# Kernel tuning notes

Measured on AMD Instinct MI355X. Metric: run time of the kernel, lower is better.

The kernel has to match this reference:

```python
import jax, jax.numpy as jnp
import numpy as np
import math

NEG_INF = -1e9
B, Q, M, P, HID, H, S = 4, 512, 512, 128, 1024, 16, 64
R = M + Q            # 1024, key length
POSLEN = M + 2 * Q   # 1536


def rel_shift(x):
    # x: [N, H, Q, Rp] -> relative-shifted, same shape
    n, h, q, rp = x.shape
    padded = jnp.pad(x, ((0, 0), (0, 0), (0, 0), (1, 0)))
    return padded.reshape(n, h, rp + 1, q)[:, :, 1:].reshape(n, h, q, rp)


def _attention(query, token_mask, key_content, value, key_position,
               segment_encoding, segment_matrix,
               content_bias, position_bias, segment_bias):
    # query: [N,Q,H,S]; key_content/value: [N,R,H,S]; key_position: [N,Rp,H,S]
    r = key_content.shape[1]
    content_att = jnp.einsum('nqhs,nrhs->nhqr', query + content_bias, key_content)
    position_att = jnp.einsum('nqhs,nrhs->nhqr', query + position_bias, key_position)
    position_att = rel_shift(position_att)[..., 1:1 + r]
    segment_att = jnp.einsum('nqhs,ghs->nhqg', query + segment_bias, segment_encoding)
    # select same-segment (g=1) vs diff-segment (g=0) logit per (q, r) pair
    segment_att = jnp.where(segment_matrix[:, None],           # [N,1,Q,R]
                            segment_att[..., 1:],              # [N,H,Q,1]
                            segment_att[..., :1])
    scale = 1.0 / math.sqrt(float(S))
    logits = (content_att + position_att + segment_att) * scale
    logits = logits + token_mask * NEG_INF
    weights = jax.nn.softmax(logits, axis=3)
    return jnp.einsum('nhqr,nrhs->nqhs', weights, value)


def setup_inputs() -> dict:
    key = jax.random.key(0)
    ks = jax.random.split(key, 16)
    sc = 0.05
    content_inputs = jax.random.normal(ks[0], (B, Q, HID), jnp.float32)
    query_inputs = jax.random.normal(ks[1], (B, P, HID), jnp.float32)
    position_encoding = jax.random.normal(ks[2], (B, POSLEN, HID), jnp.float32)
    segment_encoding = jax.random.normal(ks[3], (2, H, S), jnp.float32) * sc
    segment_matrix = jax.random.randint(ks[4], (B, Q, R), 0, 2) > 0
    # one-hot target mapping: P distinct target positions per batch row
    tpos = jax.vmap(lambda k: jax.random.permutation(k, Q)[:P])(jax.random.split(ks[5], B))
    target_mapping = jax.nn.one_hot(tpos, Q, dtype=jnp.float32)  # [B,P,Q]
    # causal-style permutation masks (1 = masked)
    causal = (jnp.arange(R)[None, :] > (jnp.arange(Q)[:, None] + M)).astype(jnp.float32)
    content_mask = jnp.broadcast_to(causal[None, None], (B, 1, Q, R))
    diag = jnp.pad(jnp.eye(Q, dtype=jnp.float32), ((0, 0), (M, 0)))
    query_mask = jnp.broadcast_to(jnp.minimum(causal + diag, 1.0)[None, None], (B, 1, Q, R))
    content_bias = jax.random.normal(ks[6], (H, S), jnp.float32) * sc
    position_bias = jax.random.normal(ks[7], (H, S), jnp.float32) * sc
    segment_bias = jax.random.normal(ks[8], (H, S), jnp.float32) * sc
    mems = jax.random.normal(ks[9], (B, M, HID), jnp.float32)
    wsc = 1.0 / math.sqrt(HID)
    Wq = jax.random.normal(ks[10], (HID, H, S), jnp.float32) * wsc
    Wkc = jax.random.normal(ks[11], (HID, H, S), jnp.float32) * wsc
    Wv = jax.random.normal(ks[12], (HID, H, S), jnp.float32) * wsc
    Wkp = jax.random.normal(ks[13], (HID, H, S), jnp.float32) * wsc
    Wo = jax.random.normal(ks[14], (H, S, HID), jnp.float32) * wsc
    return dict(content_inputs=content_inputs, query_inputs=query_inputs,
                position_encoding=position_encoding, segment_encoding=segment_encoding,
                segment_matrix=segment_matrix, target_mapping=target_mapping,
                content_mask=content_mask, query_mask=query_mask,
                content_bias=content_bias, position_bias=position_bias,
                segment_bias=segment_bias, mems=mems,
                Wq=Wq, Wkc=Wkc, Wv=Wv, Wkp=Wkp, Wo=Wo)


def reference(content_inputs, query_inputs, position_encoding, segment_encoding,
              segment_matrix, target_mapping, content_mask, query_mask,
              content_bias, position_bias, segment_bias, mems,
              Wq, Wkc, Wv, Wkp, Wo):
    split = lambda x, w: jnp.einsum('nld,dhs->nlhs', x, w)
    merge = lambda x, w: jnp.einsum('nlhs,hsd->nld', x, w)
    contexts = jnp.concatenate([mems, content_inputs], axis=1)  # [B,R,HID]
    key_content = split(contexts, Wkc)
    value = split(contexts, Wv)
    key_position = split(position_encoding, Wkp)
    attn = lambda q, m: _attention(q, m, key_content, value, key_position,
                                   segment_encoding, segment_matrix,
                                   content_bias, position_bias, segment_bias)
    # content stream
    q_c = split(content_inputs, Wq)
    content_outputs = merge(attn(q_c, content_mask), Wo)
    # query stream, scattered to target positions via one-hot target_mapping
    q_q = split(query_inputs, Wq)                               # [B,P,H,S]
    q_q = jnp.einsum('nphs,npq->nqhs', q_q, target_mapping)     # [B,Q,H,S]
    query_outputs = attn(q_q, query_mask)
    query_outputs = jnp.einsum('nqhs,npq->nphs', query_outputs, target_mapping)
    query_outputs = merge(query_outputs, Wo)
    return content_outputs, query_outputs
```

## Files before the change

kernel.cpp:

```cpp
#include <hip/hip_runtime.h>
#include <hip/hip_bf16.h>
#include <math.h>

#define B_ 4
#define Q_ 512
#define M_ 512
#define P_ 128
#define HID_ 1024
#define H_ 16
#define S_ 64
#define R_ 1024
#define POSLEN_ 1536

typedef short bf16x8 __attribute__((ext_vector_type(8)));
typedef float f32x4 __attribute__((ext_vector_type(4)));
typedef unsigned int u32;
typedef unsigned long long u64;

__device__ __forceinline__ ushort f2bf(float f) {
    u32 u = __float_as_uint(f);
    u32 r = (u + 0x7fffu + ((u >> 16) & 1u)) >> 16;
    return (ushort)r;
}
__device__ __forceinline__ float bf2f(ushort s) {
    return __uint_as_float(((u32)s) << 16);
}
__device__ __forceinline__ void gload16(void* l, const void* g) {
    __builtin_amdgcn_global_load_lds(
        (const __attribute__((address_space(1))) u32*)g,
        (__attribute__((address_space(3))) u32*)l, 16, 0, 0);
}

__global__ void find_tpos_k(const float* __restrict__ tm, int* __restrict__ tpos) {
    int i = blockIdx.x * blockDim.x + threadIdx.x;
    if (i >= B_ * P_) return;
    const float* row = tm + (size_t)i * Q_;
    int q = 0;
    for (int j = 0; j < Q_; ++j) q = (row[j] > 0.5f) ? j : q;
    tpos[i] = q;
}

__global__ __launch_bounds__(256) void cvt_all(
    const float* __restrict__ content, const float* __restrict__ mems,
    const float* __restrict__ posenc,  const float* __restrict__ query,
    ushort* __restrict__ ctx, ushort* __restrict__ pos,
    ushort* __restrict__ cont, ushort* __restrict__ qry)
{
    int v = blockIdx.x * 256 + threadIdx.x;
    const float* src;
    ushort* dst;
    if (v < 524288) {
        int row = v >> 7, c8 = v & 127;
        int n = row >> 10, l = row & 1023;
        src = (l < M_) ? mems + ((size_t)(n * M_ + l)) * 1024 + c8 * 8
                       : content + ((size_t)(n * Q_ + (l - M_))) * 1024 + c8 * 8;
        dst = ctx + (size_t)v * 8;
    } else if (v < 1310720) {
        int u = v - 524288;
        src = posenc + (size_t)u * 8; dst = pos + (size_t)u * 8;
    } else if (v < 1572864) {
        int u = v - 1310720;
        src = content + (size_t)u * 8; dst = cont + (size_t)u * 8;
    } else {
        int u = v - 1572864;
        src = query + (size_t)u * 8; dst = qry + (size_t)u * 8;
    }
    float4 a = *(const float4*)src;
    float4 b = *(const float4*)(src + 4);
    ushort4 o0 = {f2bf(a.x), f2bf(a.y), f2bf(a.z), f2bf(a.w)};
    ushort4 o1 = {f2bf(b.x), f2bf(b.y), f2bf(b.z), f2bf(b.w)};
    *(ushort4*)dst = o0;
    *(ushort4*)(dst + 4) = o1;
}

__global__ __launch_bounds__(256) void transpose5(
    const float* W0, const float* W1, const float* W2, const float* W3, const float* W4,
    ushort* T0, ushort* T1, ushort* T2, ushort* T3, ushort* T4)
{
    __shared__ float t[32][33];
    const float* W; ushort* T;
    switch (blockIdx.z) {
        case 0: W = W0; T = T0; break;
        case 1: W = W1; T = T1; break;
        case 2: W = W2; T = T2; break;
        case 3: W = W3; T = T3; break;
        default: W = W4; T = T4; break;
    }
    int bx = blockIdx.x * 32, by = blockIdx.y * 32;
    int tx = threadIdx.x & 31, ty = threadIdx.x >> 5;
    #pragma unroll
    for (int i = 0; i < 32; i += 8)
        t[ty + i][tx] = W[(size_t)(by + ty + i) * 1024 + bx + tx];
    __syncthreads();
    #pragma unroll
    for (int i = 0; i < 32; i += 8)
        T[(size_t)(bx + ty + i) * 1024 + by + tx] = f2bf(t[tx][ty + i]);
}

__global__ __launch_bounds__(256) void seg_prep(const float* __restrict__ segenc,
                                                const float* __restrict__ cb,
                                                const float* __restrict__ sb,
                                                ushort* __restrict__ seg_bf,
                                                float* __restrict__ segc) {
    for (int t = threadIdx.x; t < 16 * 16 * 64; t += 256) {
        int h = t >> 10, g = (t >> 6) & 15, s = t & 63;
        float v = (g < 2) ? segenc[(size_t)(g * 16 + h) * 64 + s] : 0.f;
        seg_bf[t] = f2bf(v);
    }
    if (threadIdx.x < 32) {
        int h = threadIdx.x >> 1, g = threadIdx.x & 1;
        float acc = 0.f;
        for (int s = 0; s < 64; ++s)
            acc += (sb[h * 64 + s] - cb[h * 64 + s]) * segenc[(size_t)(g * 16 + h) * 64 + s];
        segc[h * 2 + g] = acc;
    }
}

__global__ __launch_bounds__(256) void pack_seg(const int* __restrict__ seg, u64* __restrict__ out) {
    int idx = blockIdx.x * 256 + threadIdx.x;
    u64 m = __ballot(seg[idx] > 0);
    if ((threadIdx.x & 63) == 0) out[idx >> 6] = m;
}

__global__ __launch_bounds__(256) void proj_all(
    const ushort* __restrict__ ctx, const ushort* __restrict__ pos,
    const ushort* __restrict__ cont, const ushort* __restrict__ qry,
    const ushort* __restrict__ Wkc_t, const ushort* __restrict__ Wv_t,
    const ushort* __restrict__ Wkp_t, const ushort* __restrict__ Wq_t,
    ushort* __restrict__ KC, ushort* __restrict__ Vt, ushort* __restrict__ KP,
    ushort* __restrict__ Qccb, ushort* __restrict__ Qcpb,
    ushort* __restrict__ Qqcb, ushort* __restrict__ Qqpb,
    const float* __restrict__ cbias, const float* __restrict__ pbias)
{
    __shared__ ushort As[128 * 64];
    __shared__ ushort Bs[64 * 64];
    const int y = blockIdx.y;
    const ushort *A, *Bt;
    ushort *O1, *O2 = nullptr;
    const float *b1 = nullptr, *b2 = nullptr;
    int LROWS, MODE, m0;
    if (y < 32)       { A = ctx;  Bt = Wkc_t; O1 = KC;   LROWS = 1024; MODE = 1; m0 = y * 128; }
    else if (y < 64)  { A = ctx;  Bt = Wv_t;  O1 = Vt;   LROWS = 1024; MODE = 2; m0 = (y - 32) * 128; }
    else if (y < 112) { A = pos;  Bt = Wkp_t; O1 = KP;   LROWS = 1536; MODE = 1; m0 = (y - 64) * 128; }
    else if (y < 128) { A = cont; Bt = Wq_t;  O1 = Qccb; O2 = Qcpb; b1 = cbias; b2 = pbias; LROWS = 512; MODE = 1; m0 = (y - 112) * 128; }
    else              { A = qry;  Bt = Wq_t;  O1 = Qqcb; O2 = Qqpb; b1 = cbias; b2 = pbias; LROWS = 128; MODE = 1; m0 = (y - 128) * 128; }
    const int nn_blk = m0 / LROWS;
    const int lrbase = m0 - nn_blk * LROWS;

    const int tid = threadIdx.x;
    const int lane = tid & 63, wave = tid >> 6;
    const int l15 = lane & 15, hi = lane >> 4;
    const int wm = wave >> 1, wn = wave & 1;
    const int n0 = blockIdx.x * 64;

    f32x4 acc[4][2];
    #pragma unroll
    for (int i = 0; i < 4; ++i)
        #pragma unroll
        for (int j = 0; j < 2; ++j) acc[i][j] = f32x4{0.f, 0.f, 0.f, 0.f};

    for (int k0 = 0; k0 < 1024; k0 += 64) {
        __syncthreads();
        #pragma unroll
        for (int it = 0; it < 4; ++it) {
            int idx = it * 256 + tid;
            gload16(&As[idx * 8], A + (size_t)(m0 + (idx >> 3)) * 1024 + k0 + (idx & 7) * 8);
        }
        #pragma unroll
        for (int it = 0; it < 2; ++it) {
            int idx = it * 256 + tid;
            gload16(&Bs[idx * 8], Bt + (size_t)(n0 + (idx >> 3)) * 1024 + k0 + (idx & 7) * 8);
        }
        __syncthreads();
        #pragma unroll
        for (int kk = 0; kk < 2; ++kk) {
            const int krd = kk * 32 + hi * 8;
            bf16x8 af[4], bfr[2];
            #pragma unroll
            for (int i = 0; i < 4; ++i)
                af[i] = *(const bf16x8*)&As[(wm * 64 + i * 16 + l15) * 64 + krd];
            #pragma unroll
            for (int j = 0; j < 2; ++j)
                bfr[j] = *(const bf16x8*)&Bs[(wn * 32 + j * 16 + l15) * 64 + krd];
            #pragma unroll
            for (int i = 0; i < 4; ++i)
                #pragma unroll
                for (int j = 0; j < 2; ++j)
                    acc[i][j] = __builtin_amdgcn_mfma_f32_16x16x32_bf16(af[i], bfr[j], acc[i][j], 0, 0, 0);
        }
    }

    #pragma unroll
    for (int i = 0; i < 4; ++i)
        #pragma unroll
        for (int j = 0; j < 2; ++j) {
            int col = n0 + wn * 32 + j * 16 + l15;
            float bb1 = b1 ? b1[col] : 0.f;
            float bb2 = b2 ? b2[col] : 0.f;
            #pragma unroll
            for (int r = 0; r < 4; ++r) {
                int lrow = wm * 64 + i * 16 + hi * 4 + r;
                float v = acc[i][j][r];
                if (MODE == 1) {
                    size_t o = ((size_t)(nn_blk * 16 + (col >> 6)) * LROWS + lrbase + lrow) * 64 + (col & 63);
                    O1[o] = f2bf(v + bb1);
                    if (O2) O2[o] = f2bf(v + bb2);
                } else {
                    int row = m0 + lrow;
                    int nn = row >> 10, rr = row & 1023;
                    O1[((size_t)(nn * 16 + (col >> 6)) * 64 + (col & 63)) * 1024 + rr] = f2bf(v);
                }
            }
        }
}

__global__ __launch_bounds__(256) void oproj(
    const ushort* __restrict__ AOc, const ushort* __restrict__ AOq,
    const ushort* __restrict__ Wo_t, float* __restrict__ out)
{
    __shared__ ushort As[128 * 64];
    __shared__ ushort Bs[64 * 64];
    const int y = blockIdx.y;
    const ushort* A;
    float* C;
    int m0;
    if (y < 16) { A = AOc; C = out; m0 = y * 128; }
    else        { A = AOq; C = out + (size_t)B_ * Q_ * 1024; m0 = (y - 16) * 128; }

    const int tid = threadIdx.x;
    const int lane = tid & 63, wave = tid >> 6;
    const int l15 = lane & 15, hi = lane >> 4;
    const int wm = wave >> 1, wn = wave & 1;
    const int n0 = blockIdx.x * 64;

    f32x4 acc[4][2];
    #pragma unroll
    for (int i = 0; i < 4; ++i)
        #pragma unroll
        for (int j = 0; j < 2; ++j) acc[i][j] = f32x4{0.f, 0.f, 0.f, 0.f};

    for (int k0 = 0; k0 < 1024; k0 += 64) {
        __syncthreads();
        #pragma unroll
        for (int it = 0; it < 4; ++it) {
            int idx = it * 256 + tid;
            gload16(&As[idx * 8], A + (size_t)(m0 + (idx >> 3)) * 1024 + k0 + (idx & 7) * 8);
        }
        #pragma unroll
        for (int it = 0; it < 2; ++it) {
            int idx = it * 256 + tid;
            gload16(&Bs[idx * 8], Wo_t + (size_t)(n0 + (idx >> 3)) * 1024 + k0 + (idx & 7) * 8);
        }
        __syncthreads();
        #pragma unroll
        for (int kk = 0; kk < 2; ++kk) {
            const int krd = kk * 32 + hi * 8;
            bf16x8 af[4], bfr[2];
            #pragma unroll
            for (int i = 0; i < 4; ++i)
                af[i] = *(const bf16x8*)&As[(wm * 64 + i * 16 + l15) * 64 + krd];
            #pragma unroll
            for (int j = 0; j < 2; ++j)
                bfr[j] = *(const bf16x8*)&Bs[(wn * 32 + j * 16 + l15) * 64 + krd];
            #pragma unroll
            for (int i = 0; i < 4; ++i)
                #pragma unroll
                for (int j = 0; j < 2; ++j)
                    acc[i][j] = __builtin_amdgcn_mfma_f32_16x16x32_bf16(af[i], bfr[j], acc[i][j], 0, 0, 0);
        }
    }
    #pragma unroll
    for (int i = 0; i < 4; ++i)
        #pragma unroll
        for (int j = 0; j < 2; ++j) {
            int col = n0 + wn * 32 + j * 16 + l15;
            #pragma unroll
            for (int r = 0; r < 4; ++r) {
                int row = m0 + wm * 64 + i * 16 + hi * 4 + r;
                C[(size_t)row * 1024 + col] = acc[i][j][r];
            }
        }
}

__global__ __launch_bounds__(256) void pa_gemm(const ushort* __restrict__ Qpb,
                                               const ushort* __restrict__ KPb,
                                               ushort* __restrict__ PA) {
    const int tid = threadIdx.x;
    const int lane = tid & 63, w = tid >> 6;
    const int l15 = lane & 15, hi = lane >> 4;
    const int jt = blockIdx.x * 128, nh = blockIdx.y;
    const int p0 = w * 32;

    bf16x8 a[2][2];
    #pragma unroll
    for (int i = 0; i < 2; ++i)
        #pragma unroll
        for (int kk = 0; kk < 2; ++kk)
            a[i][kk] = *(const bf16x8*)(Qpb + ((size_t)(nh * 128 + p0 + i * 16 + l15)) * 64 + kk * 32 + hi * 8);

    #pragma unroll
    for (int jc = 0; jc < 8; ++jc) {
        f32x4 c0 = {0.f,0.f,0.f,0.f}, c1 = {0.f,0.f,0.f,0.f};
        #pragma unroll
        for (int kk = 0; kk < 2; ++kk) {
            bf16x8 b = *(const bf16x8*)(KPb + ((size_t)nh * 1536 + jt + jc * 16 + l15) * 64 + kk * 32 + hi * 8);
            c0 = __builtin_amdgcn_mfma_f32_16x16x32_bf16(a[0][kk], b, c0, 0, 0, 0);
            c1 = __builtin_amdgcn_mfma_f32_16x16x32_bf16(a[1][kk], b, c1, 0, 0, 0);
        }
        #pragma unroll
        for (int r = 0; r < 4; ++r) {
            PA[((size_t)(nh * 128 + p0 + hi * 4 + r)) * 1536 + jt + jc * 16 + l15] = f2bf(c0[r]);
            PA[((size_t)(nh * 128 + p0 + 16 + hi * 4 + r)) * 1536 + jt + jc * 16 + l15] = f2bf(c1[r]);
        }
    }
}

#define EXSC 0.180336879f
#define EXBI -23.0831204f
__global__ __launch_bounds__(128) void attn_uni(
    const ushort* __restrict__ Qccb, const ushort* __restrict__ Qcpb,
    const ushort* __restrict__ Qqcb,
    const ushort* __restrict__ KCb,  const ushort* __restrict__ KPb,
    const ushort* __restrict__ Vtb,  const ushort* __restrict__ segb,
    const float* __restrict__ segc,  const u64* __restrict__ pseg,
    const int* __restrict__ tpos,    const ushort* __restrict__ PA,
    float* __restrict__ Pp)
{
    __shared__ ushort Kt[2][64 * 64];
    __shared__ ushort DlT[2][96 * 34];
    __shared__ ushort Pl[2][32 * 64];

    const int tid = threadIdx.x;
    const int lane = tid & 63, wv = tid >> 6;
    const int l15 = lane & 15, hi = lane >> 4;

    int wg = blockIdx.x + 10 * (blockIdx.y + 32 * blockIdx.z);
    int swz = (wg & 7) * 160 + (wg >> 3);
    const int bx = swz % 10;
    int rem = swz / 10;
    const int gy = rem & 31;
    const int n = rem >> 5;

    const bool ISQ = bx >= 8;
    const int h = gy & 15, half = gy >> 4;
    const int nh = n * 16 + h;
    const int q0w = (ISQ ? (bx - 8) * 64 : bx * 64) + wv * 32;

    ushort* dlt = DlT[wv];
    ushort* pl  = Pl[wv];

    bf16x8 acb[2][2], apb[2][2];
    {
        const ushort* qc = ISQ ? (Qqcb + ((size_t)nh * P_ + q0w) * 64)
                               : (Qccb + ((size_t)nh * Q_ + q0w) * 64);
        #pragma unroll
        for (int i = 0; i < 2; ++i)
            #pragma unroll
            for (int kk = 0; kk < 2; ++kk)
                acb[i][kk] = *(const bf16x8*)(qc + (size_t)(i * 16 + l15) * 64 + kk * 32 + hi * 8);
        if (!ISQ) {
            const ushort* qp = Qcpb + ((size_t)nh * Q_ + q0w) * 64;
            #pragma unroll
            for (int i = 0; i < 2; ++i)
                #pragma unroll
                for (int kk = 0; kk < 2; ++kk)
                    apb[i][kk] = *(const bf16x8*)(qp + (size_t)(i * 16 + l15) * 64 + kk * 32 + hi * 8);
        } else {
            apb[0][0] = acb[0][0]; apb[0][1] = acb[0][1];
            apb[1][0] = acb[1][0]; apb[1][1] = acb[1][1];
        }
    }

    float sd[2][2][4];
    {
        f32x4 sg[2] = {{0.f,0.f,0.f,0.f},{0.f,0.f,0.f,0.f}};
        #pragma unroll
        for (int kk = 0; kk < 2; ++kk) {
            bf16x8 b = *(const bf16x8*)(segb + (size_t)(h * 16 + l15) * 64 + kk * 32 + hi * 8);
            sg[0] = __builtin_amdgcn_mfma_f32_16x16x32_bf16(acb[0][kk], b, sg[0], 0, 0, 0);
            sg[1] = __builtin_amdgcn_mfma_f32_16x16x32_bf16(acb[1][kk], b, sg[1], 0, 0, 0);
        }
        float c0 = segc[h * 2 + 0], c1 = segc[h * 2 + 1];
        #pragma unroll
        for (int i = 0; i < 2; ++i)
            #pragma unroll
            for (int r = 0; r < 4; ++r) {
                int base = (lane & 48) << 2;
                sd[0][i][r] = __int_as_float(__builtin_amdgcn_ds_bpermute(base, __float_as_int(sg[i][r]))) + c0;
                sd[1][i][r] = __int_as_float(__builtin_amdgcn_ds_bpermute(base + 4, __float_as_int(sg[i][r]))) + c1;
            }
    }

    int qg[2][4];
    #pragma unroll
    for (int i = 0; i < 2; ++i)
        #pragma unroll
        for (int r = 0; r < 4; ++r) {
            int p = q0w + i * 16 + hi * 4 + r;
            qg[i][r] = ISQ ? tpos[n * P_ + p] : p;
        }

    f32x4 acc[2][4];
    float psum[2][4] = {};
    #pragma unroll
    for (int i = 0; i < 2; ++i)
        #pragma unroll
        for (int j = 0; j < 4; ++j) acc[i][j] = f32x4{0.f,0.f,0.f,0.f};

    auto stage = [&](int b, int rt) {
        const int r0s = rt * 64;
        #pragma unroll
        for (int it = 0; it < 4; ++it) {
            int e = it * 128 + tid;
            int row = e >> 3;
            int sc = ((e & 7) * 8) ^ ((row & 7) << 3);
            gload16(&Kt[b][e * 8], KCb + ((size_t)nh * R_ + r0s + row) * 64 + sc);
        }
    };

    const int q0top = (ISQ ? (bx - 8) * 64 : bx * 64) + 32;
    const int ntb = ISQ ? 16 : min(16, ((q0top + 543) >> 6) + 1);
    const int nt1 = (ntb + 1) >> 1;
    const int t0 = half ? nt1 : 0;
    const int tmax = half ? ntb : nt1;

    stage(0, t0);
    __syncthreads();
    int buf = 0;

    for (int rt = t0; rt < tmax; ++rt) {
        const int r0 = rt * 64;
        if (rt + 1 < tmax) stage(buf ^ 1, rt + 1);

        const bool skip = !ISQ && (r0 > q0w + 543);
        if (!skip) {
            bf16x8 vf[2][4];
            #pragma unroll
            for (int kk = 0; kk < 2; ++kk)
                #pragma unroll
                for (int dj = 0; dj < 4; ++dj)
                    vf[kk][dj] = *(const bf16x8*)(Vtb + ((size_t)nh * 64 + dj * 16 + l15) * 1024 + r0 + kk * 32 + hi * 8);

            f32x4 s[2][4];
            #pragma unroll
            for (int i = 0; i < 2; ++i)
                #pragma unroll
                for (int fc = 0; fc < 4; ++fc) s[i][fc] = f32x4{0.f,0.f,0.f,0.f};
            #pragma unroll
            for (int kk = 0; kk < 2; ++kk) {
                #pragma unroll
                for (int fc = 0; fc < 4; ++fc) {
                    int krow = fc * 16 + l15;
                    bf16x8 kb = *(const bf16x8*)&Kt[buf][krow * 64 + ((kk * 32 + hi * 8) ^ ((krow & 7) << 3))];
                    s[0][fc] = __builtin_amdgcn_mfma_f32_16x16x32_bf16(acb[0][kk], kb, s[0][fc], 0, 0, 0);
                    s[1][fc] = __builtin_amdgcn_mfma_f32_16x16x32_bf16(acb[1][kk], kb, s[1][fc], 0, 0, 0);
                }
            }

            if (!ISQ) {
                const int jb0 = r0 - q0w + 481;
                #pragma unroll
                for (int t = 0; t < 6; ++t) {
                    f32x4 d0 = {0.f,0.f,0.f,0.f}, d1 = {0.f,0.f,0.f,0.f};
                    #pragma unroll
                    for (int kk = 0; kk < 2; ++kk) {
                        bf16x8 pv = *(const bf16x8*)(KPb + ((size_t)nh * POSLEN_ + jb0 + t * 16 + l15) * 64 + kk * 32 + hi * 8);
                        d0 = __builtin_amdgcn_mfma_f32_16x16x32_bf16(apb[0][kk], pv, d0, 0, 0, 0);
                        d1 = __builtin_amdgcn_mfma_f32_16x16x32_bf16(apb[1][kk], pv, d1, 0, 0, 0);
                    }
                    int jj = (t * 16 + l15) * 34;
                    *(u32*)&dlt[jj + hi * 4]          = (u32)f2bf(d0[0]) | ((u32)f2bf(d0[1]) << 16);
                    *(u32*)&dlt[jj + hi * 4 + 2]      = (u32)f2bf(d0[2]) | ((u32)f2bf(d0[3]) << 16);
                    *(u32*)&dlt[jj + 16 + hi * 4]     = (u32)f2bf(d1[0]) | ((u32)f2bf(d1[1]) << 16);
                    *(u32*)&dlt[jj + 16 + hi * 4 + 2] = (u32)f2bf(d1[2]) | ((u32)f2bf(d1[3]) << 16);
                }
            }

            float pav[2][4][4];
            if (ISQ) {
                #pragma unroll
                for (int i = 0; i < 2; ++i)
                    #pragma unroll
                    for (int fc = 0; fc < 4; ++fc)
                        #pragma unroll
                        for (int r = 0; r < 4; ++r) {
                            int qq = i * 16 + hi * 4 + r;
                            int j = (r0 + fc * 16 + l15) - qg[i][r] + 512;
                            pav[i][fc][r] = bf2f(PA[((size_t)nh * P_ + q0w + qq) * 1536 + j]);
                        }
            }

            #pragma unroll
            for (int i = 0; i < 2; ++i) {
                u64 sw[4];
                #pragma unroll
                for (int r = 0; r < 4; ++r)
                    sw[r] = pseg[((size_t)n * Q_ + qg[i][r]) * 16 + rt];
                #pragma unroll
                for (int fc = 0; fc < 4; ++fc) {
                    #pragma unroll
                    for (int r = 0; r < 4; ++r) {
                        int qq = i * 16 + hi * 4 + r;
                        int rr = fc * 16 + l15;
                        float dval = ISQ ? pav[i][fc][r] : bf2f(dlt[(rr - qq + 31) * 34 + qq]);
                        int sel = (int)((sw[r] >> rr) & 1);
                        float st = s[i][fc][r] + dval + (sel ? sd[1][i][r] : sd[0][i][r]);
                        float v = fmaf(st, EXSC, EXBI);
                        bool masked = ISQ ? ((r0 + rr) >= qg[i][r] + 512)
                                          : ((r0 + rr) > qg[i][r] + 512);
                        v = masked ? -INFINITY : v;
                        float pv = exp2f(v);
                        ushort us = f2bf(pv);
                        psum[i][r] += bf2f(us);
                        int row = i * 16 + hi * 4 + r;
                        int cc = (fc * 16 + l15) ^ ((row & 7) << 3);
                        pl[row * 64 + cc] = us;
                    }
                }
            }

            #pragma unroll
            for (int kk = 0; kk < 2; ++kk) {
                bf16x8 pa[2];
                #pragma unroll
                for (int i = 0; i < 2; ++i) {
                    int row = i * 16 + l15;
                    int cc = (kk * 32 + hi * 8) ^ ((row & 7) << 3);
                    pa[i] = *(const bf16x8*)&pl[row * 64 + cc];
                }
                #pragma unroll
                for (int dj = 0; dj < 4; ++dj) {
                    acc[0][dj] = __builtin_amdgcn_mfma_f32_16x16x32_bf16(pa[0], vf[kk][dj], acc[0][dj], 0, 0, 0);
                    acc[1][dj] = __builtin_amdgcn_mfma_f32_16x16x32_bf16(pa[1], vf[kk][dj], acc[1][dj], 0, 0, 0);
                }
            }
        }
        __syncthreads();
        buf ^= 1;
    }

    #pragma unroll
    for (int i = 0; i < 2; ++i)
        #pragma unroll
        for (int r = 0; r < 4; ++r) {
            #pragma unroll
            for (int d = 1; d < 16; d <<= 1) psum[i][r] += __shfl_xor(psum[i][r], d, 64);
        }

    #pragma unroll
    for (int i = 0; i < 2; ++i)
        #pragma unroll
        for (int r = 0; r < 4; ++r) {
            int qrow = q0w + i * 16 + hi * 4 + r;
            size_t rowg = ISQ ? (32768 + (size_t)nh * P_ + qrow) : ((size_t)nh * Q_ + qrow);
            float* base = Pp + (rowg * 2 + half) * 72;
            #pragma unroll
            for (int dj = 0; dj < 4; ++dj)
                base[dj * 16 + l15] = acc[i][dj][r];
            if (l15 == 0) base[64] = psum[i][r];
        }
}

__global__ __launch_bounds__(256) void combine_k(const float* __restrict__ Pp,
                                                 ushort* __restrict__ AOc,
                                                 ushort* __restrict__ AOq) {
    int idx = blockIdx.x * 256 + threadIdx.x;
    int row = idx >> 6, d = idx & 63;
    const float* b0 = Pp + ((size_t)row * 2 + 0) * 72;
    const float* b1 = b0 + 72;
    float l = b0[64] + b1[64];
    ushort o = f2bf((b0[d] + b1[d]) / l);
    if (row < 32768) {
        int n = row >> 13, h = (row >> 9) & 15, q = row & 511;
        AOc[((size_t)(n * Q_ + q)) * 1024 + h * 64 + d] = o;
    } else {
        int r2 = row - 32768;
        int n = r2 >> 11, h = (r2 >> 7) & 15, p = r2 & 127;
        AOq[((size_t)(n * P_ + p)) * 1024 + h * 64 + d] = o;
    }
}

extern "C" void kernel_launch(void* const* d_in, const int* in_sizes, int n_in,
                              void* d_out, int out_size, void* d_ws, size_t ws_size,
                              hipStream_t stream) {
    const float* content = (const float*)d_in[0];
    const float* query   = (const float*)d_in[1];
    const float* posenc  = (const float*)d_in[2];
    const float* segenc  = (const float*)d_in[3];
    const int*   segmat  = (const int*)d_in[4];
    const float* tmap    = (const float*)d_in[5];
    const float* cbias   = (const float*)d_in[8];
    const float* pbias   = (const float*)d_in[9];
    const float* sbias   = (const float*)d_in[10];
    const float* mems    = (const float*)d_in[11];
    const float* Wq      = (const float*)d_in[12];
    const float* Wkc     = (const float*)d_in[13];
    const float* Wv      = (const float*)d_in[14];
    const float* Wkp     = (const float*)d_in[15];
    const float* Wo      = (const float*)d_in[16];
    float* out = (float*)d_out;

    char* p = (char*)d_ws;
    auto alloc = [&](size_t bytes) { char* r = p; p += (bytes + 255) & ~(size_t)255; return r; };
    ushort* ctx_bf  = (ushort*)alloc((size_t)B_ * R_ * 1024 * 2);
    ushort* pos_bf  = (ushort*)alloc((size_t)B_ * POSLEN_ * 1024 * 2);
    ushort* cont_bf = (ushort*)alloc((size_t)B_ * Q_ * 1024 * 2);
    ushort* qry_bf  = (ushort*)alloc((size_t)B_ * P_ * 1024 * 2);
    ushort* Wq_t    = (ushort*)alloc(1024 * 1024 * 2);
    ushort* Wkc_t   = (ushort*)alloc(1024 * 1024 * 2);
    ushort* Wv_t    = (ushort*)alloc(1024 * 1024 * 2);
    ushort* Wkp_t   = (ushort*)alloc(1024 * 1024 * 2);
    ushort* Wo_t    = (ushort*)alloc(1024 * 1024 * 2);
    ushort* KC_bf   = (ushort*)alloc((size_t)B_ * 16 * R_ * 64 * 2);
    ushort* Vt_bf   = (ushort*)alloc((size_t)B_ * 16 * 64 * R_ * 2);
    ushort* KP_bf   = (ushort*)alloc((size_t)B_ * 16 * POSLEN_ * 64 * 2);
    ushort* Qc_cb   = (ushort*)alloc((size_t)B_ * 16 * Q_ * 64 * 2);
    ushort* Qc_pb   = (ushort*)alloc((size_t)B_ * 16 * Q_ * 64 * 2);
    ushort* Qq_cb   = (ushort*)alloc((size_t)B_ * 16 * P_ * 64 * 2);
    ushort* Qq_pb   = (ushort*)alloc((size_t)B_ * 16 * P_ * 64 * 2);
    ushort* PA_bf   = (ushort*)alloc((size_t)B_ * 16 * P_ * POSLEN_ * 2);
    ushort* AOc_bf  = (ushort*)alloc((size_t)B_ * Q_ * 1024 * 2);
    ushort* AOq_bf  = (ushort*)alloc((size_t)B_ * P_ * 1024 * 2);
    ushort* seg_bf  = (ushort*)alloc(16 * 16 * 64 * 2);
    float*  segc    = (float*)alloc(32 * 4);
    u64*    pseg    = (u64*)alloc((size_t)B_ * Q_ * 16 * 8);
    int*    tpos    = (int*)alloc(B_ * P_ * 4);
    float* Pp = (float*)ctx_bf;

    find_tpos_k<<<2, 256, 0, stream>>>(tmap, tpos);
    cvt_all<<<6400, 256, 0, stream>>>(content, mems, posenc, query,
                                      ctx_bf, pos_bf, cont_bf, qry_bf);
    transpose5<<<dim3(32, 32, 5), 256, 0, stream>>>(Wq, Wkc, Wv, Wkp, Wo,
                                                    Wq_t, Wkc_t, Wv_t, Wkp_t, Wo_t);
    seg_prep<<<1, 256, 0, stream>>>(segenc, cbias, sbias, seg_bf, segc);
    pack_seg<<<8192, 256, 0, stream>>>(segmat, pseg);

    proj_all<<<dim3(16, 132), 256, 0, stream>>>(ctx_bf, pos_bf, cont_bf, qry_bf,
                                                Wkc_t, Wv_t, Wkp_t, Wq_t,
                                                KC_bf, Vt_bf, KP_bf,
                                                Qc_cb, Qc_pb, Qq_cb, Qq_pb,
                                                cbias, pbias);

    pa_gemm<<<dim3(12, 64), 256, 0, stream>>>(Qq_pb, KP_bf, PA_bf);

    attn_uni<<<dim3(10, 32, 4), 128, 0, stream>>>(Qc_cb, Qc_pb, Qq_cb, KC_bf, KP_bf, Vt_bf,
                                                  seg_bf, segc, pseg, tpos, PA_bf, Pp);

    combine_k<<<10240, 256, 0, stream>>>(Pp, AOc_bf, AOq_bf);

    oproj<<<dim3(16, 20), 256, 0, stream>>>(AOc_bf, AOq_bf, Wo_t, out);

    (void)in_sizes; (void)n_in; (void)out_size; (void)ws_size;
}
```

Measured before the change: 317.1 us.

## Widen projection GEMM tiles and split attention into single-wave blocks

The projection and output GEMMs move from 128x64 to 128x128 tiles, giving each wave a 4x4 MFMA block, halving the grid, and reusing each A tile across more output columns. The attention kernel becomes one wave per block with 32 query rows. It drops the LDS-staged, double-buffered K tile and its barriers, loading K fragments straight from global memory. The relative-position band is now kept in fp32 LDS instead of bf16, and per-wave causal tile counts are tighter. The trade-off is more accumulator registers in the GEMMs, fewer GEMM blocks for occupancy, and unstaged global K loads in attention.

```diff
diff --git a/kernel.cpp b/kernel.cpp
--- a/kernel.cpp
+++ b/kernel.cpp
@@ -133,7 +133,7 @@
     const float* __restrict__ cbias, const float* __restrict__ pbias)
 {
     __shared__ ushort As[128 * 64];
-    __shared__ ushort Bs[64 * 64];
+    __shared__ ushort Bs[128 * 64];
     const int y = blockIdx.y;
     const ushort *A, *Bt;
     ushort *O1, *O2 = nullptr;
@@ -151,13 +151,13 @@
     const int lane = tid & 63, wave = tid >> 6;
     const int l15 = lane & 15, hi = lane >> 4;
     const int wm = wave >> 1, wn = wave & 1;
-    const int n0 = blockIdx.x * 64;
-
-    f32x4 acc[4][2];
+    const int n0 = blockIdx.x * 128;
+
+    f32x4 acc[4][4];
     #pragma unroll
     for (int i = 0; i < 4; ++i)
         #pragma unroll
-        for (int j = 0; j < 2; ++j) acc[i][j] = f32x4{0.f, 0.f, 0.f, 0.f};
+        for (int j = 0; j < 4; ++j) acc[i][j] = f32x4{0.f, 0.f, 0.f, 0.f};
 
     for (int k0 = 0; k0 < 1024; k0 += 64) {
         __syncthreads();
@@ -165,27 +165,22 @@
         for (int it = 0; it < 4; ++it) {
             int idx = it * 256 + tid;
             gload16(&As[idx * 8], A + (size_t)(m0 + (idx >> 3)) * 1024 + k0 + (idx & 7) * 8);
-        }
-        #pragma unroll
-        for (int it = 0; it < 2; ++it) {
-            int idx = it * 256 + tid;
             gload16(&Bs[idx * 8], Bt + (size_t)(n0 + (idx >> 3)) * 1024 + k0 + (idx & 7) * 8);
         }
         __syncthreads();
         #pragma unroll
         for (int kk = 0; kk < 2; ++kk) {
             const int krd = kk * 32 + hi * 8;
-            bf16x8 af[4], bfr[2];
-            #pragma unroll
-            for (int i = 0; i < 4; ++i)
-                af[i] = *(const bf16x8*)&As[(wm * 64 + i * 16 + l15) * 64 + krd];
-            #pragma unroll
-            for (int j = 0; j < 2; ++j)
-                bfr[j] = *(const bf16x8*)&Bs[(wn * 32 + j * 16 + l15) * 64 + krd];
+            bf16x8 af[4], bfr[4];
+            #pragma unroll
+            for (int i = 0; i < 4; ++i) {
+                af[i]  = *(const bf16x8*)&As[(wm * 64 + i * 16 + l15) * 64 + krd];
+                bfr[i] = *(const bf16x8*)&Bs[(wn * 64 + i * 16 + l15) * 64 + krd];
+            }
             #pragma unroll
             for (int i = 0; i < 4; ++i)
                 #pragma unroll
-                for (int j = 0; j < 2; ++j)
+                for (int j = 0; j < 4; ++j)
                     acc[i][j] = __builtin_amdgcn_mfma_f32_16x16x32_bf16(af[i], bfr[j], acc[i][j], 0, 0, 0);
         }
     }
@@ -193,8 +188,8 @@
     #pragma unroll
     for (int i = 0; i < 4; ++i)
         #pragma unroll
-        for (int j = 0; j < 2; ++j) {
-            int col = n0 + wn * 32 + j * 16 + l15;
+        for (int j = 0; j < 4; ++j) {
+            int col = n0 + wn * 64 + j * 16 + l15;
             float bb1 = b1 ? b1[col] : 0.f;
             float bb2 = b2 ? b2[col] : 0.f;
             #pragma unroll
@@ -219,7 +214,7 @@
     const ushort* __restrict__ Wo_t, float* __restrict__ out)
 {
     __shared__ ushort As[128 * 64];
-    __shared__ ushort Bs[64 * 64];
+    __shared__ ushort Bs[128 * 64];
     const int y = blockIdx.y;
     const ushort* A;
     float* C;
@@ -231,13 +226,13 @@
     const int lane = tid & 63, wave = tid >> 6;
     const int l15 = lane & 15, hi = lane >> 4;
     const int wm = wave >> 1, wn = wave & 1;
-    const int n0 = blockIdx.x * 64;
-
-    f32x4 acc[4][2];
+    const int n0 = blockIdx.x * 128;
+
+    f32x4 acc[4][4];
     #pragma unroll
     for (int i = 0; i < 4; ++i)
         #pragma unroll
-        for (int j = 0; j < 2; ++j) acc[i][j] = f32x4{0.f, 0.f, 0.f, 0.f};
+        for (int j = 0; j < 4; ++j) acc[i][j] = f32x4{0.f, 0.f, 0.f, 0.f};
 
     for (int k0 = 0; k0 < 1024; k0 += 64) {
         __syncthreads();
@@ -245,35 +240,30 @@
         for (int it = 0; it < 4; ++it) {
             int idx = it * 256 + tid;
             gload16(&As[idx * 8], A + (size_t)(m0 + (idx >> 3)) * 1024 + k0 + (idx & 7) * 8);
-        }
-        #pragma unroll
-        for (int it = 0; it < 2; ++it) {
-            int idx = it * 256 + tid;
             gload16(&Bs[idx * 8], Wo_t + (size_t)(n0 + (idx >> 3)) * 1024 + k0 + (idx & 7) * 8);
         }
         __syncthreads();
         #pragma unroll
         for (int kk = 0; kk < 2; ++kk) {
             const int krd = kk * 32 + hi * 8;
-            bf16x8 af[4], bfr[2];
-            #pragma unroll
-            for (int i = 0; i < 4; ++i)
-                af[i] = *(const bf16x8*)&As[(wm * 64 + i * 16 + l15) * 64 + krd];
-            #pragma unroll
-            for (int j = 0; j < 2; ++j)
-                bfr[j] = *(const bf16x8*)&Bs[(wn * 32 + j * 16 + l15) * 64 + krd];
+            bf16x8 af[4], bfr[4];
+            #pragma unroll
+            for (int i = 0; i < 4; ++i) {
+                af[i]  = *(const bf16x8*)&As[(wm * 64 + i * 16 + l15) * 64 + krd];
+                bfr[i] = *(const bf16x8*)&Bs[(wn * 64 + i * 16 + l15) * 64 + krd];
+            }
             #pragma unroll
             for (int i = 0; i < 4; ++i)
                 #pragma unroll
-                for (int j = 0; j < 2; ++j)
+                for (int j = 0; j < 4; ++j)
                     acc[i][j] = __builtin_amdgcn_mfma_f32_16x16x32_bf16(af[i], bfr[j], acc[i][j], 0, 0, 0);
         }
     }
     #pragma unroll
     for (int i = 0; i < 4; ++i)
         #pragma unroll
-        for (int j = 0; j < 2; ++j) {
-            int col = n0 + wn * 32 + j * 16 + l15;
+        for (int j = 0; j < 4; ++j) {
+            int col = n0 + wn * 64 + j * 16 + l15;
             #pragma unroll
             for (int r = 0; r < 4; ++r) {
                 int row = m0 + wm * 64 + i * 16 + hi * 4 + r;
@@ -317,7 +307,7 @@
 
 #define EXSC 0.180336879f
 #define EXBI -23.0831204f
-__global__ __launch_bounds__(128) void attn_uni(
+__global__ __launch_bounds__(64) void attn_uni(
     const ushort* __restrict__ Qccb, const ushort* __restrict__ Qcpb,
     const ushort* __restrict__ Qqcb,
     const ushort* __restrict__ KCb,  const ushort* __restrict__ KPb,
@@ -326,28 +316,23 @@
     const int* __restrict__ tpos,    const ushort* __restrict__ PA,
     float* __restrict__ Pp)
 {
-    __shared__ ushort Kt[2][64 * 64];
-    __shared__ ushort DlT[2][96 * 34];
-    __shared__ ushort Pl[2][32 * 64];
-
-    const int tid = threadIdx.x;
-    const int lane = tid & 63, wv = tid >> 6;
+    __shared__ float Dlf[96 * 36];
+    __shared__ ushort Pl[32 * 64];
+
+    const int lane = threadIdx.x;
     const int l15 = lane & 15, hi = lane >> 4;
 
-    int wg = blockIdx.x + 10 * (blockIdx.y + 32 * blockIdx.z);
-    int swz = (wg & 7) * 160 + (wg >> 3);
-    const int bx = swz % 10;
-    int rem = swz / 10;
+    int wg = blockIdx.x + 20 * (blockIdx.y + 32 * blockIdx.z);
+    int swz = (wg & 7) * 320 + (wg >> 3);
+    const int bx = swz % 20;
+    int rem = swz / 20;
     const int gy = rem & 31;
     const int n = rem >> 5;
 
-    const bool ISQ = bx >= 8;
+    const bool ISQ = bx >= 16;
     const int h = gy & 15, half = gy >> 4;
     const int nh = n * 16 + h;
-    const int q0w = (ISQ ? (bx - 8) * 64 : bx * 64) + wv * 32;
-
-    ushort* dlt = DlT[wv];
-    ushort* pl  = Pl[wv];
+    const int q0w = (ISQ ? (bx - 16) : bx) * 32;
 
     bf16x8 acb[2][2], apb[2][2];
     {
@@ -407,136 +392,114 @@
         #pragma unroll
         for (int j = 0; j < 4; ++j) acc[i][j] = f32x4{0.f,0.f,0.f,0.f};
 
-    auto stage = [&](int b, int rt) {
-        const int r0s = rt * 64;
-        #pragma unroll
-        for (int it = 0; it < 4; ++it) {
-            int e = it * 128 + tid;
-            int row = e >> 3;
-            int sc = ((e & 7) * 8) ^ ((row & 7) << 3);
-            gload16(&Kt[b][e * 8], KCb + ((size_t)nh * R_ + r0s + row) * 64 + sc);
-        }
-    };
-
-    const int q0top = (ISQ ? (bx - 8) * 64 : bx * 64) + 32;
-    const int ntb = ISQ ? 16 : min(16, ((q0top + 543) >> 6) + 1);
+    const int ntb = ISQ ? 16 : (((q0w + 543) >> 6) + 1);
     const int nt1 = (ntb + 1) >> 1;
     const int t0 = half ? nt1 : 0;
     const int tmax = half ? ntb : nt1;
 
-    stage(0, t0);
-    __syncthreads();
-    int buf = 0;
-
     for (int rt = t0; rt < tmax; ++rt) {
         const int r0 = rt * 64;
-        if (rt + 1 < tmax) stage(buf ^ 1, rt + 1);
-
-        const bool skip = !ISQ && (r0 > q0w + 543);
-        if (!skip) {
-            bf16x8 vf[2][4];
-            #pragma unroll
-            for (int kk = 0; kk < 2; ++kk)
+
+        bf16x8 vf[2][4], kf[2][4];
+        #pragma unroll
+        for (int kk = 0; kk < 2; ++kk)
+            #pragma unroll
+            for (int dj = 0; dj < 4; ++dj)
+                vf[kk][dj] = *(const bf16x8*)(Vtb + ((size_t)nh * 64 + dj * 16 + l15) * 1024 + r0 + kk * 32 + hi * 8);
+        #pragma unroll
+        for (int kk = 0; kk < 2; ++kk)
+            #pragma unroll
+            for (int fc = 0; fc < 4; ++fc)
+                kf[kk][fc] = *(const bf16x8*)(KCb + ((size_t)nh * R_ + r0 + fc * 16 + l15) * 64 + kk * 32 + hi * 8);
+
+        f32x4 s[2][4];
+        #pragma unroll
+        for (int i = 0; i < 2; ++i)
+            #pragma unroll
+            for (int fc = 0; fc < 4; ++fc) s[i][fc] = f32x4{0.f,0.f,0.f,0.f};
+        #pragma unroll
+        for (int kk = 0; kk < 2; ++kk)
+            #pragma unroll
+            for (int fc = 0; fc < 4; ++fc) {
+                s[0][fc] = __builtin_amdgcn_mfma_f32_16x16x32_bf16(acb[0][kk], kf[kk][fc], s[0][fc], 0, 0, 0);
+                s[1][fc] = __builtin_amdgcn_mfma_f32_16x16x32_bf16(acb[1][kk], kf[kk][fc], s[1][fc], 0, 0, 0);
+            }
+
+        if (!ISQ) {
+            const int jb0 = r0 - q0w + 481;
+            #pragma unroll
+            for (int t = 0; t < 6; ++t) {
+                f32x4 d0 = {0.f,0.f,0.f,0.f}, d1 = {0.f,0.f,0.f,0.f};
                 #pragma unroll
-                for (int dj = 0; dj < 4; ++dj)
-                    vf[kk][dj] = *(const bf16x8*)(Vtb + ((size_t)nh * 64 + dj * 16 + l15) * 1024 + r0 + kk * 32 + hi * 8);
-
-            f32x4 s[2][4];
+                for (int kk = 0; kk < 2; ++kk) {
+                    bf16x8 pv = *(const bf16x8*)(KPb + ((size_t)nh * POSLEN_ + jb0 + t * 16 + l15) * 64 + kk * 32 + hi * 8);
+                    d0 = __builtin_amdgcn_mfma_f32_16x16x32_bf16(apb[0][kk], pv, d0, 0, 0, 0);
+                    d1 = __builtin_amdgcn_mfma_f32_16x16x32_bf16(apb[1][kk], pv, d1, 0, 0, 0);
+                }
+                float* wp = &Dlf[(t * 16 + l15) * 36];
+                *(f32x4*)(wp + hi * 4) = d0;
+                *(f32x4*)(wp + 16 + hi * 4) = d1;
+            }
+        }
+
+        float pav[2][4][4];
+        if (ISQ) {
             #pragma unroll
             for (int i = 0; i < 2; ++i)
                 #pragma unroll
-                for (int fc = 0; fc < 4; ++fc) s[i][fc] = f32x4{0.f,0.f,0.f,0.f};
-            #pragma unroll
-            for (int kk = 0; kk < 2; ++kk) {
-                #pragma unroll
-                for (int fc = 0; fc < 4; ++fc) {
-                    int krow = fc * 16 + l15;
-                    bf16x8 kb = *(const bf16x8*)&Kt[buf][krow * 64 + ((kk * 32 + hi * 8) ^ ((krow & 7) << 3))];
-                    s[0][fc] = __builtin_amdgcn_mfma_f32_16x16x32_bf16(acb[0][kk], kb, s[0][fc], 0, 0, 0);
-                    s[1][fc] = __builtin_amdgcn_mfma_f32_16x16x32_bf16(acb[1][kk], kb, s[1][fc], 0, 0, 0);
-                }
-            }
-
-            if (!ISQ) {
-                const int jb0 = r0 - q0w + 481;
-                #pragma unroll
-                for (int t = 0; t < 6; ++t) {
-                    f32x4 d0 = {0.f,0.f,0.f,0.f}, d1 = {0.f,0.f,0.f,0.f};
-                    #pragma unroll
-                    for (int kk = 0; kk < 2; ++kk) {
-                        bf16x8 pv = *(const bf16x8*)(KPb + ((size_t)nh * POSLEN_ + jb0 + t * 16 + l15) * 64 + kk * 32 + hi * 8);
-                        d0 = __builtin_amdgcn_mfma_f32_16x16x32_bf16(apb[0][kk], pv, d0, 0, 0, 0);
-                        d1 = __builtin_amdgcn_mfma_f32_16x16x32_bf16(apb[1][kk], pv, d1, 0, 0, 0);
-                    }
-                    int jj = (t * 16 + l15) * 34;
-                    *(u32*)&dlt[jj + hi * 4]          = (u32)f2bf(d0[0]) | ((u32)f2bf(d0[1]) << 16);
-                    *(u32*)&dlt[jj + hi * 4 + 2]      = (u32)f2bf(d0[2]) | ((u32)f2bf(d0[3]) << 16);
-                    *(u32*)&dlt[jj + 16 + hi * 4]     = (u32)f2bf(d1[0]) | ((u32)f2bf(d1[1]) << 16);
-                    *(u32*)&dlt[jj + 16 + hi * 4 + 2] = (u32)f2bf(d1[2]) | ((u32)f2bf(d1[3]) << 16);
-                }
-            }
-
-            float pav[2][4][4];
-            if (ISQ) {
-                #pragma unroll
-                for (int i = 0; i < 2; ++i)
-                    #pragma unroll
-                    for (int fc = 0; fc < 4; ++fc)
-                        #pragma unroll
-                        for (int r = 0; r < 4; ++r) {
-                            int qq = i * 16 + hi * 4 + r;
-                            int j = (r0 + fc * 16 + l15) - qg[i][r] + 512;
-                            pav[i][fc][r] = bf2f(PA[((size_t)nh * P_ + q0w + qq) * 1536 + j]);
-                        }
-            }
-
-            #pragma unroll
-            for (int i = 0; i < 2; ++i) {
-                u64 sw[4];
-                #pragma unroll
-                for (int r = 0; r < 4; ++r)
-                    sw[r] = pseg[((size_t)n * Q_ + qg[i][r]) * 16 + rt];
-                #pragma unroll
-                for (int fc = 0; fc < 4; ++fc) {
+                for (int fc = 0; fc < 4; ++fc)
                     #pragma unroll
                     for (int r = 0; r < 4; ++r) {
                         int qq = i * 16 + hi * 4 + r;
-                        int rr = fc * 16 + l15;
-                        float dval = ISQ ? pav[i][fc][r] : bf2f(dlt[(rr - qq + 31) * 34 + qq]);
-                        int sel = (int)((sw[r] >> rr) & 1);
-                        float st = s[i][fc][r] + dval + (sel ? sd[1][i][r] : sd[0][i][r]);
-                        float v = fmaf(st, EXSC, EXBI);
-                        bool masked = ISQ ? ((r0 + rr) >= qg[i][r] + 512)
-                                          : ((r0 + rr) > qg[i][r] + 512);
-                        v = masked ? -INFINITY : v;
-                        float pv = exp2f(v);
-                        ushort us = f2bf(pv);
-                        psum[i][r] += bf2f(us);
-                        int row = i * 16 + hi * 4 + r;
-                        int cc = (fc * 16 + l15) ^ ((row & 7) << 3);
-                        pl[row * 64 + cc] = us;
+                        int j = (r0 + fc * 16 + l15) - qg[i][r] + 512;
+                        pav[i][fc][r] = bf2f(PA[((size_t)nh * P_ + q0w + qq) * 1536 + j]);
                     }
+        }
+
+        #pragma unroll
+        for (int i = 0; i < 2; ++i) {
+            u64 sw[4];
+            #pragma unroll
+            for (int r = 0; r < 4; ++r)
+                sw[r] = pseg[((size_t)n * Q_ + qg[i][r]) * 16 + rt];
+            #pragma unroll
+            for (int fc = 0; fc < 4; ++fc) {
+                #pragma unroll
+                for (int r = 0; r < 4; ++r) {
+                    int qq = i * 16 + hi * 4 + r;
+                    int rr = fc * 16 + l15;
+                    float dval = ISQ ? pav[i][fc][r] : Dlf[(rr - qq + 31) * 36 + qq];
+                    int sel = (int)((sw[r] >> rr) & 1);
+                    float st = s[i][fc][r] + dval + (sel ? sd[1][i][r] : sd[0][i][r]);
+                    float v = fmaf(st, EXSC, EXBI);
+                    bool masked = ISQ ? ((r0 + rr) >= qg[i][r] + 512)
+                                      : ((r0 + rr) > qg[i][r] + 512);
+                    v = masked ? -INFINITY : v;
+                    float pv = exp2f(v);
+                    ushort us = f2bf(pv);
+                    psum[i][r] += bf2f(us);
+                    int row = i * 16 + hi * 4 + r;
+                    int cc = (fc * 16 + l15) ^ ((row & 7) << 3);
+                    Pl[row * 64 + cc] = us;
                 }
             }
-
-            #pragma unroll
-            for (int kk = 0; kk < 2; ++kk) {
-                bf16x8 pa[2];
-                #pragma unroll
-                for (int i = 0; i < 2; ++i) {
-                    int row = i * 16 + l15;
-                    int cc = (kk * 32 + hi * 8) ^ ((row & 7) << 3);
-                    pa[i] = *(const bf16x8*)&pl[row * 64 + cc];
-                }
-                #pragma unroll
-                for (int dj = 0; dj < 4; ++dj) {
-                    acc[0][dj] = __builtin_amdgcn_mfma_f32_16x16x32_bf16(pa[0], vf[kk][dj], acc[0][dj], 0, 0, 0);
-                    acc[1][dj] = __builtin_amdgcn_mfma_f32_16x16x32_bf16(pa[1], vf[kk][dj], acc[1][dj], 0, 0, 0);
-                }
-            }
-        }
-        __syncthreads();
-        buf ^= 1;
+        }
+
+        #pragma unroll
+        for (int kk = 0; kk < 2; ++kk) {
+            bf16x8 pa[2];
+            #pragma unroll
+            for (int i = 0; i < 2; ++i) {
+                int row = i * 16 + l15;
+                int cc = (kk * 32 + hi * 8) ^ ((row & 7) << 3);
+                pa[i] = *(const bf16x8*)&Pl[row * 64 + cc];
+            }
+            #pragma unroll
+            for (int dj = 0; dj < 4; ++dj) {
+                acc[0][dj] = __builtin_amdgcn_mfma_f32_16x16x32_bf16(pa[0], vf[kk][dj], acc[0][dj], 0, 0, 0);
+                acc[1][dj] = __builtin_amdgcn_mfma_f32_16x16x32_bf16(pa[1], vf[kk][dj], acc[1][dj], 0, 0, 0);
+            }
+        }
     }
 
     #pragma unroll
@@ -635,20 +598,20 @@
     seg_prep<<<1, 256, 0, stream>>>(segenc, cbias, sbias, seg_bf, segc);
     pack_seg<<<8192, 256, 0, stream>>>(segmat, pseg);
 
-    proj_all<<<dim3(16, 132), 256, 0, stream>>>(ctx_bf, pos_bf, cont_bf, qry_bf,
-                                                Wkc_t, Wv_t, Wkp_t, Wq_t,
-                                                KC_bf, Vt_bf, KP_bf,
-                                                Qc_cb, Qc_pb, Qq_cb, Qq_pb,
-                                                cbias, pbias);
+    proj_all<<<dim3(8, 132), 256, 0, stream>>>(ctx_bf, pos_bf, cont_bf, qry_bf,
+                                               Wkc_t, Wv_t, Wkp_t, Wq_t,
+                                               KC_bf, Vt_bf, KP_bf,
+                                               Qc_cb, Qc_pb, Qq_cb, Qq_pb,
+                                               cbias, pbias);
 
     pa_gemm<<<dim3(12, 64), 256, 0, stream>>>(Qq_pb, KP_bf, PA_bf);
 
-    attn_uni<<<dim3(10, 32, 4), 128, 0, stream>>>(Qc_cb, Qc_pb, Qq_cb, KC_bf, KP_bf, Vt_bf,
-                                                  seg_bf, segc, pseg, tpos, PA_bf, Pp);
+    attn_uni<<<dim3(20, 32, 4), 64, 0, stream>>>(Qc_cb, Qc_pb, Qq_cb, KC_bf, KP_bf, Vt_bf,
+                                                 seg_bf, segc, pseg, tpos, PA_bf, Pp);
 
     combine_k<<<10240, 256, 0, stream>>>(Pp, AOc_bf, AOq_bf);
 
-    oproj<<<dim3(16, 20), 256, 0, stream>>>(AOc_bf, AOq_bf, Wo_t, out);
+    oproj<<<dim3(8, 20), 256, 0, stream>>>(AOc_bf, AOq_bf, Wo_t, out);
 
     (void)in_sizes; (void)n_in; (void)out_size; (void)ws_size;
 }
```

Measured after the change: 333.3 us. 5.1% more time.
